# Optimization experiments

Hardware: AMD Instinct MI355X
Metric: run time of the kernel (lower is better)

Reference implementation:

```python
import jax, jax.numpy as jnp
import numpy as np

B, N, E, DIN = 2048, 38, 4, 9
H0, H1, L0 = 256, 256, 512
EPS = 1e-5
_mask_np = np.ones((N, DIN), np.float32)
_mask_np[np.arange(0, N, 2), :] = 0.0
MASK = jnp.asarray(_mask_np)  # (N, DIN); masked rows zeroed


def _bn_relu(h, g, b):
    # h: (B, N, 1, D); BatchNorm2d(N) normalizes over (batch, H=1, W=D) per node channel
    mu = jnp.mean(h, axis=(0, 2, 3), keepdims=True)
    var = jnp.var(h, axis=(0, 2, 3), keepdims=True)  # biased var, as torch BN
    h = (h - mu) * jax.lax.rsqrt(var + EPS) * g[None, :, None, None] + b[None, :, None, None]
    return jax.nn.relu(h)


def _gconv(adj, nodes, Ws, bs, We, be):
    # adj: (B, E, N, N); nodes: (B, N, 1, Din)
    out = Ws.shape[0]
    hs = nodes @ Ws.T + bs  # self term: (B, N, 1, out)
    m = (nodes @ We.T + be).reshape(nodes.shape[0], N, out, E)
    hr = jnp.einsum('bemn,bnce->bmc', adj, m)  # relational aggregation
    return hs + hr[:, :, None, :]


def _forward(adj, x, cWs0, cbs0, cWe0, cbe0, cg0, cb0, cWs1, cbs1, cWe1, cbe1, cg1, cb1, lW0, lb0, lg0, lbb0, fW, fb):
    masked_x = MASK * x
    h = masked_x[:, :, None, :]
    h = _bn_relu(_gconv(adj, h, cWs0, cbs0, cWe0, cbe0), cg0, cb0)
    h = _bn_relu(_gconv(adj, h, cWs1, cbs1, cWe1, cbe1), cg1, cb1)
    h = _bn_relu(h @ lW0.T + lb0, lg0, lbb0)
    h = (h @ fW.T + fb)[:, :, 0, :]  # (B, N, 2*DIN)
    s_logits, t = h[..., :DIN], h[..., DIN:]
    s = jax.nn.sigmoid(s_logits)
    out = masked_x + (1.0 - MASK) * (x + t) * s
    logdet = jnp.sum(jax.nn.log_sigmoid(s_logits).reshape(x.shape[0], -1), axis=1)
    return out, logdet


def setup_inputs() -> dict:
    key = jax.random.key(0)
    ks = jax.random.split(key, 8)
    rn = lambda k, shape: jax.random.normal(ks[k], shape, jnp.float32) * 0.1
    return {
        'adj': jax.random.uniform(ks[0], (B, E, N, N), jnp.float32),
        'x': jax.random.normal(ks[1], (B, N, DIN), jnp.float32),
        'cWs0': rn(2, (H0, DIN)), 'cbs0': jnp.zeros((H0,), jnp.float32),
        'cWe0': rn(3, (H0 * E, DIN)), 'cbe0': jnp.zeros((H0 * E,), jnp.float32),
        'cg0': jnp.ones((N,), jnp.float32), 'cb0': jnp.zeros((N,), jnp.float32),
        'cWs1': rn(4, (H1, H0)), 'cbs1': jnp.zeros((H1,), jnp.float32),
        'cWe1': rn(5, (H1 * E, H0)), 'cbe1': jnp.zeros((H1 * E,), jnp.float32),
        'cg1': jnp.ones((N,), jnp.float32), 'cb1': jnp.zeros((N,), jnp.float32),
        'lW0': rn(6, (L0, H1)), 'lb0': jnp.zeros((L0,), jnp.float32),
        'lg0': jnp.ones((N,), jnp.float32), 'lbb0': jnp.zeros((N,), jnp.float32),
        'fW': rn(7, (2 * DIN, L0)), 'fb': jnp.zeros((2 * DIN,), jnp.float32),
    }


def reference(adj, x, cWs0, cbs0, cWe0, cbe0, cg0, cb0, cWs1, cbs1, cWe1, cbe1, cg1, cb1, lW0, lb0, lg0, lbb0, fW, fb):
    return _forward(adj, x, cWs0, cbs0, cWe0, cbe0, cg0, cb0, cWs1, cbs1, cWe1, cbe1, cg1, cb1, lW0, lb0, lg0, lbb0, fW, fb)
```

## Files before the change

### kernel.cpp

```cpp
#include <hip/hip_runtime.h>
#include <hip/hip_bf16.h>
#include <math.h>

#define B_   2048
#define N_   38
#define E_   4
#define DIN_ 9
#define H0_  256
#define H1_  256
#define L0_  512
#define M_   (B_ * N_)

typedef short bf16x8 __attribute__((ext_vector_type(8)));
typedef float f32x4 __attribute__((ext_vector_type(4)));

__device__ __forceinline__ float b2f(unsigned short u) {
  return __uint_as_float((unsigned)u << 16);
}
__device__ __forceinline__ unsigned short f2b(float f) {
  __hip_bfloat16 h = __float2bfloat16(f);
  return *(unsigned short*)&h;
}

__device__ __forceinline__ float rsum16(float v) {
  v += __shfl_xor(v, 1);
  v += __shfl_xor(v, 2);
  v += __shfl_xor(v, 4);
  v += __shfl_xor(v, 8);
  return v;
}

__global__ void k_build_wg0(const float* __restrict__ Ws, const float* __restrict__ bs,
                            const float* __restrict__ We, const float* __restrict__ be,
                            unsigned short* __restrict__ WT) {
  int i = blockIdx.x * 256 + threadIdx.x;
  if (i >= 256 * 96) return;
  int c = i / 96, k = i % 96;
  float v = 0.f;
  if (k < 64) {
    int e = k >> 4, f = k & 15;
    if (f < 9) v = We[(c * 4 + e) * 9 + f];
    else if (f == 9) v = be[c * 4 + e];
  } else if (k < 80) {
    int f = k - 64;
    if (f < 9) v = Ws[c * 9 + f];
    else if (f == 9) v = bs[c];
  }
  WT[i] = f2b(v);
}

__global__ void k_build_wcat(const float* __restrict__ Ws, const float* __restrict__ We,
                             unsigned short* __restrict__ WT) {
  int i = blockIdx.x * 256 + threadIdx.x;
  if (i >= 256 * 1280) return;
  int c = i / 1280, k = i % 1280;
  float v;
  if (k < 256) v = Ws[c * 256 + k];
  else { int kk = k - 256; int e = kk >> 8, f = kk & 255; v = We[(c * 4 + e) * 256 + f]; }
  WT[i] = f2b(v);
}

__global__ void k_build_wl(const float* __restrict__ W, unsigned short* __restrict__ WT) {
  int i = blockIdx.x * 256 + threadIdx.x;
  if (i >= 512 * 256) return;
  WT[i] = f2b(W[i]);
}

__global__ void k_build_wf(const float* __restrict__ W, unsigned short* __restrict__ WT) {
  int i = blockIdx.x * 256 + threadIdx.x;
  if (i >= 32 * 512) return;
  int r = i / 512, k = i % 512;
  WT[i] = f2b(r < 18 ? W[r * 512 + k] : 0.f);
}

__global__ __launch_bounds__(256) void k_gred(const float* __restrict__ part, int nblk,
                                              float* __restrict__ st) {
  const int j = blockIdx.x, tid = threadIdx.x;
  float s = 0.f;
  for (int i = tid; i < nblk; i += 256) s += part[(size_t)i * 76 + j];
#pragma unroll
  for (int off = 32; off; off >>= 1) s += __shfl_down(s, off);
  __shared__ float r[4];
  if ((tid & 63) == 0) r[tid >> 6] = s;
  __syncthreads();
  if (tid == 0) {
    float tot = r[0] + r[1] + r[2] + r[3];
    if (j < 38) st[j * 2] = tot;
    else st[(j - 38) * 2 + 1] = tot;
  }
}

__global__ __launch_bounds__(256) void k_gconv0(
    const float* __restrict__ adj, const float* __restrict__ x,
    const unsigned short* __restrict__ Wg0, unsigned short* __restrict__ g,
    float* __restrict__ part) {
  __shared__ __align__(16) unsigned short adjB[4 * 48 * 64];
  __shared__ __align__(16) unsigned short zB[48 * 64];
  __shared__ __align__(16) unsigned short xLA[64 * 32];
  __shared__ __align__(16) unsigned short xLB[16 * 64];
  __shared__ float lsumW[4][48], lsqW[4][48];
  const int b = blockIdx.x, t = threadIdx.x;
  const uint4 z4 = make_uint4(0, 0, 0, 0);
  for (int i = t; i < 4 * 48 * 64 / 8; i += 256) ((uint4*)adjB)[i] = z4;
  for (int i = t; i < 64 * 32 / 8; i += 256) ((uint4*)xLA)[i] = z4;
  for (int i = t; i < 16 * 64 / 8; i += 256) ((uint4*)xLB)[i] = z4;
  __syncthreads();
  for (int i = t; i < 4 * 38 * 38; i += 256) {
    int e = i / 1444, r = i % 1444, m = r / 38, n = r % 38;
    adjB[(e * 48 + m) * 64 + n] = f2b(adj[(size_t)b * 5776 + i]);
  }
  for (int i = t; i < 342; i += 256) {
    int m = i / 9, f = i % 9;
    float v = x[(size_t)b * 342 + i];
    unsigned short bv = f2b((m & 1) ? v : 0.f);
    xLA[m * 32 + f] = bv;
    xLB[f * 64 + m] = bv;
  }
  if (t < 38) {
    unsigned short one = f2b(1.f);
    xLA[t * 32 + 9] = one;
    xLB[9 * 64 + t] = one;
  }
  __syncthreads();
  const int w = t >> 6, L = t & 63;
  const int lrow = L & 15, quad = L >> 4;
  {
    f32x4 za[3];
#pragma unroll
    for (int mt = 0; mt < 3; ++mt) za[mt] = (f32x4){0.f, 0.f, 0.f, 0.f};
#pragma unroll
    for (int kk = 0; kk < 2; ++kk) {
      bf16x8 bb = *(const bf16x8*)&xLB[lrow * 64 + kk * 32 + quad * 8];
#pragma unroll
      for (int mt = 0; mt < 3; ++mt) {
        bf16x8 aa = *(const bf16x8*)&adjB[(w * 48 + mt * 16 + lrow) * 64 + kk * 32 + quad * 8];
        za[mt] = __builtin_amdgcn_mfma_f32_16x16x32_bf16(aa, bb, za[mt], 0, 0, 0);
      }
    }
#pragma unroll
    for (int mt = 0; mt < 3; ++mt)
#pragma unroll
      for (int reg = 0; reg < 4; ++reg)
        zB[(mt * 16 + quad * 4 + reg) * 64 + w * 16 + lrow] = f2b(za[mt][reg]);
  }
  __syncthreads();
  f32x4 acc[3][4];
#pragma unroll
  for (int mt = 0; mt < 3; ++mt)
#pragma unroll
    for (int nt = 0; nt < 4; ++nt) acc[mt][nt] = (f32x4){0.f, 0.f, 0.f, 0.f};
#pragma unroll
  for (int kc = 0; kc < 3; ++kc) {
    bf16x8 af[3];
#pragma unroll
    for (int mt = 0; mt < 3; ++mt)
      af[mt] = (kc < 2)
                   ? *(const bf16x8*)&zB[(mt * 16 + lrow) * 64 + kc * 32 + quad * 8]
                   : *(const bf16x8*)&xLA[(mt * 16 + lrow) * 32 + quad * 8];
#pragma unroll
    for (int nt = 0; nt < 4; ++nt) {
      const int c = w * 64 + nt * 16 + lrow;
      bf16x8 bf_ = *(const bf16x8*)&Wg0[(size_t)c * 96 + kc * 32 + quad * 8];
#pragma unroll
      for (int mt = 0; mt < 3; ++mt)
        acc[mt][nt] = __builtin_amdgcn_mfma_f32_16x16x32_bf16(af[mt], bf_, acc[mt][nt], 0, 0, 0);
    }
  }
#pragma unroll
  for (int mt = 0; mt < 3; ++mt) {
#pragma unroll
    for (int reg = 0; reg < 4; ++reg) {
      const int m = mt * 16 + quad * 4 + reg;
      float sv = 0.f, qv = 0.f;
      if (m < N_) {
#pragma unroll
        for (int nt = 0; nt < 4; ++nt) {
          const int c = w * 64 + nt * 16 + lrow;
          float v = acc[mt][nt][reg];
          g[((size_t)b * N_ + m) * 256 + c] = f2b(v);
          sv += v;
          qv += v * v;
        }
      }
      sv = rsum16(sv);
      qv = rsum16(qv);
      if (lrow == 0) { lsumW[w][m] = sv; lsqW[w][m] = qv; }
    }
  }
  __syncthreads();
  if (t < 38) {
    part[(size_t)b * 76 + t] = lsumW[0][t] + lsumW[1][t] + lsumW[2][t] + lsumW[3][t];
    part[(size_t)b * 76 + 38 + t] = lsqW[0][t] + lsqW[1][t] + lsqW[2][t] + lsqW[3][t];
  }
}

__global__ __launch_bounds__(256) void k_l1f(
    const float* __restrict__ adj, const unsigned short* __restrict__ g0,
    const unsigned short* __restrict__ Wcat, const float* __restrict__ st0,
    const float* __restrict__ gam, const float* __restrict__ bet,
    const float* __restrict__ bs, const float* __restrict__ be,
    unsigned short* __restrict__ h2, float* __restrict__ part) {
  __shared__ __align__(16) unsigned short adjB[4 * 48 * 64];
  __shared__ __align__(16) unsigned short Abt[256 * 48 + 16];
  __shared__ __align__(16) unsigned short Pbuf[48 * 256];
  __shared__ float aS[38], bS[38];
  __shared__ float arowS[4 * 48];
  __shared__ float lsumW[4][48], lsqW[4][48];
  const int b = blockIdx.x, t = threadIdx.x;
  for (int i = t; i < 4 * 48 * 64 / 8; i += 256) ((uint4*)adjB)[i] = make_uint4(0, 0, 0, 0);
  if (t < 38) {
    const float cnt = 2048.f * 256.f;
    float mu = st0[t * 2] / cnt;
    float var = st0[t * 2 + 1] / cnt - mu * mu;
    float a = rsqrtf(var + 1e-5f) * gam[t];
    aS[t] = a;
    bS[t] = bet[t] - mu * a;
  }
  __syncthreads();
  for (int i = t; i < 4 * 38 * 38; i += 256) {
    int e = i / 1444, r = i % 1444, m = r / 38, n = r % 38;
    *(unsigned short*)((char*)adjB + (e * 48 + m) * 128 + ((2 * n) ^ ((m & 7) << 4))) =
        f2b(adj[(size_t)b * 5776 + i]);
  }
  for (int i = t; i < 38 * 32; i += 256) {
    int n = i >> 5, seg = (i & 31) * 8;
    uint4 u = *(const uint4*)&g0[((size_t)b * N_ + n) * 256 + seg];
    float a = aS[n], bb2 = bS[n];
    unsigned* up = (unsigned*)&u;
    uint4 o;
    unsigned* op = (unsigned*)&o;
#pragma unroll
    for (int j = 0; j < 4; ++j) {
      float lo = fmaxf(fmaf(b2f((unsigned short)(up[j] & 0xffff)), a, bb2), 0.f);
      float hi = fmaxf(fmaf(b2f((unsigned short)(up[j] >> 16)), a, bb2), 0.f);
      op[j] = (unsigned)f2b(lo) | ((unsigned)f2b(hi) << 16);
    }
    *(uint4*)((char*)Pbuf + n * 512 + ((seg * 2) ^ ((n & 7) << 4))) = o;
  }
  for (int i = t; i < 10 * 32; i += 256) {
    int n = 38 + (i >> 5), seg = (i & 31) * 8;
    *(uint4*)((char*)Pbuf + n * 512 + ((seg * 2) ^ ((n & 7) << 4))) = make_uint4(0, 0, 0, 0);
  }
  __syncthreads();
  if (t < 152) {
    int e = t / 38, m = t % 38;
    float s = 0.f;
    for (int n = 0; n < 38; ++n)
      s += b2f(*(const unsigned short*)((const char*)adjB + (e * 48 + m) * 128 +
                                        ((2 * n) ^ ((m & 7) << 4))));
    arowS[e * 48 + m] = s;
  }
  {
    const int c = t;
#pragma unroll
    for (int j = 0; j < 5; ++j) {
      uint4 o;
      unsigned* op = (unsigned*)&o;
#pragma unroll
      for (int q = 0; q < 4; ++q) {
        int n0 = j * 8 + q * 2;
        unsigned short lo = 0, hi = 0;
        if (n0 < 38)
          lo = *(const unsigned short*)((const char*)Pbuf + n0 * 512 +
                                        ((2 * c) ^ ((n0 & 7) << 4)));
        if (n0 + 1 < 38)
          hi = *(const unsigned short*)((const char*)Pbuf + (n0 + 1) * 512 +
                                        ((2 * c) ^ (((n0 + 1) & 7) << 4)));
        op[q] = (unsigned)lo | ((unsigned)hi << 16);
      }
      *(uint4*)&Abt[c * 48 + j * 8] = o;
    }
    *(uint4*)&Abt[c * 48 + 40] = make_uint4(0, 0, 0, 0);
  }
  const int w = t >> 6, L = t & 63;
  const int lrow = L & 15, quad = L >> 4;
  f32x4 acc[3][4];
#pragma unroll
  for (int mt = 0; mt < 3; ++mt)
#pragma unroll
    for (int nt = 0; nt < 4; ++nt) acc[mt][nt] = (f32x4){0.f, 0.f, 0.f, 0.f};

#define MAIN_KBLOCK(WOFF)                                                              \
  _Pragma("unroll") for (int kc = 0; kc < 8; ++kc) {                                   \
    bf16x8 af[3];                                                                      \
    _Pragma("unroll") for (int mt = 0; mt < 3; ++mt) af[mt] =                          \
        *(const bf16x8*)((const char*)Pbuf + (mt * 16 + lrow) * 512 +                  \
                         ((kc * 64 + quad * 16) ^ ((lrow & 7) << 4)));                 \
    _Pragma("unroll") for (int nt = 0; nt < 4; ++nt) {                                 \
      const int c = w * 64 + nt * 16 + lrow;                                           \
      bf16x8 bf_ = *(const bf16x8*)&Wcat[(size_t)c * 1280 + (WOFF) + kc * 32 + quad * 8]; \
      _Pragma("unroll") for (int mt = 0; mt < 3; ++mt) acc[mt][nt] =                   \
          __builtin_amdgcn_mfma_f32_16x16x32_bf16(af[mt], bf_, acc[mt][nt], 0, 0, 0);  \
    }                                                                                  \
  }

  MAIN_KBLOCK(0)

#pragma unroll 1
  for (int e = 0; e < 4; ++e) {
    f32x4 pa[3][4];
#pragma unroll
    for (int mt = 0; mt < 3; ++mt)
#pragma unroll
      for (int nt = 0; nt < 4; ++nt) pa[mt][nt] = (f32x4){0.f, 0.f, 0.f, 0.f};
#pragma unroll
    for (int kk = 0; kk < 2; ++kk) {
      bf16x8 bb[4];
#pragma unroll
      for (int nt = 0; nt < 4; ++nt)
        bb[nt] = *(const bf16x8*)&Abt[(w * 64 + nt * 16 + lrow) * 48 + kk * 32 + quad * 8];
#pragma unroll
      for (int mt = 0; mt < 3; ++mt) {
        bf16x8 aa = *(const bf16x8*)((const char*)adjB + (e * 48 + mt * 16 + lrow) * 128 +
                                     ((kk * 64 + quad * 16) ^ ((lrow & 7) << 4)));
#pragma unroll
        for (int nt = 0; nt < 4; ++nt)
          pa[mt][nt] = __builtin_amdgcn_mfma_f32_16x16x32_bf16(aa, bb[nt], pa[mt][nt], 0, 0, 0);
      }
    }
    __syncthreads();
#pragma unroll
    for (int mt = 0; mt < 3; ++mt)
#pragma unroll
      for (int reg = 0; reg < 4; ++reg) {
        const int m = mt * 16 + quad * 4 + reg;
#pragma unroll
        for (int nt = 0; nt < 4; ++nt) {
          const int c2 = w * 64 + nt * 16 + lrow;
          *(unsigned short*)((char*)Pbuf + m * 512 + ((2 * c2) ^ ((m & 7) << 4))) =
              f2b(pa[mt][nt][reg]);
        }
      }
    __syncthreads();
    MAIN_KBLOCK(256 + e * 256)
  }
#undef MAIN_KBLOCK

#pragma unroll
  for (int mt = 0; mt < 3; ++mt) {
#pragma unroll
    for (int reg = 0; reg < 4; ++reg) {
      const int m = mt * 16 + quad * 4 + reg;
      float sv = 0.f, qv = 0.f;
      if (m < N_) {
        float a0 = arowS[0 * 48 + m], a1 = arowS[48 + m];
        float a2 = arowS[96 + m], a3 = arowS[144 + m];
#pragma unroll
        for (int nt = 0; nt < 4; ++nt) {
          const int col = w * 64 + nt * 16 + lrow;
          float4 bev = *(const float4*)&be[col * 4];
          float v = acc[mt][nt][reg] + bs[col] +
                    a0 * bev.x + a1 * bev.y + a2 * bev.z + a3 * bev.w;
          h2[((size_t)b * N_ + m) * 256 + col] = f2b(v);
          sv += v;
          qv += v * v;
        }
      }
      sv = rsum16(sv);
      qv = rsum16(qv);
      if (lrow == 0) { lsumW[w][m] = sv; lsqW[w][m] = qv; }
    }
  }
  __syncthreads();
  if (t < 38) {
    part[(size_t)b * 76 + t] = lsumW[0][t] + lsumW[1][t] + lsumW[2][t] + lsumW[3][t];
    part[(size_t)b * 76 + 38 + t] = lsqW[0][t] + lsqW[1][t] + lsqW[2][t] + lsqW[3][t];
  }
}

template <bool BIAS, bool STATS>
__global__ __launch_bounds__(512) void k_gemm(
    const unsigned short* __restrict__ A0, const unsigned short* __restrict__ Bw,
    const float* __restrict__ bias, const float* __restrict__ stIn,
    const float* __restrict__ gam, const float* __restrict__ bet, float cnt,
    unsigned short* __restrict__ Cout, int Cstride, float* __restrict__ part) {
  __shared__ __align__(16) unsigned short lA[128 * 32];
  __shared__ __align__(16) unsigned short lB[256 * 32];
  __shared__ float lbias[256];
  __shared__ float lsum[38], lsq[38];
  const int t = threadIdx.x;
  const int tileM = blockIdx.x, n_base = blockIdx.y * 256;
  if (BIAS && t < 256) lbias[t] = bias[n_base + t];
  if (STATS && t < 38) { lsum[t] = 0.f; lsq[t] = 0.f; }
  const int w = t >> 6, L = t & 63;
  const int wr = w >> 2, wc = w & 3;
  const int lrow = L & 15, quad = L >> 4;
  const int srow = t >> 2, sseg = (t & 3) * 8;
  const int nA = (tileM * 128 + srow) % 38;
  float aC, bC;
  {
    float mu = stIn[nA * 2] / cnt;
    float var = stIn[nA * 2 + 1] / cnt - mu * mu;
    aC = rsqrtf(var + 1e-5f) * gam[nA];
    bC = bet[nA] - mu * aC;
  }
  const unsigned short* aRow = A0 + (size_t)(tileM * 128 + srow) * 256 + sseg;
  f32x4 acc[4][4];
#pragma unroll
  for (int mt = 0; mt < 4; ++mt)
#pragma unroll
    for (int nt = 0; nt < 4; ++nt) acc[mt][nt] = (f32x4){0.f, 0.f, 0.f, 0.f};

  uint4 u = *(const uint4*)aRow;
  for (int ki = 0; ki < 8; ++ki) {
#pragma unroll
    for (int r = 0; r < 2; ++r) {
      const unsigned short* gp = Bw + (size_t)(n_base + r * 128 + srow) * 256 + ki * 32 + sseg;
      __builtin_amdgcn_global_load_lds(
          (const __attribute__((address_space(1))) void*)gp,
          (__attribute__((address_space(3))) void*)(lB + r * 4096 + w * 512), 16, 0, 0);
    }
    uint4 un = u;
    if (ki < 7) un = *(const uint4*)(aRow + (ki + 1) * 32);
    {
      uint4 o;
      unsigned* up = (unsigned*)&u;
      unsigned* op = (unsigned*)&o;
#pragma unroll
      for (int j = 0; j < 4; ++j) {
        float lo = fmaxf(fmaf(b2f((unsigned short)(up[j] & 0xffff)), aC, bC), 0.f);
        float hi = fmaxf(fmaf(b2f((unsigned short)(up[j] >> 16)), aC, bC), 0.f);
        op[j] = (unsigned)f2b(lo) | ((unsigned)f2b(hi) << 16);
      }
      *(uint4*)&lA[srow * 32 + sseg] = o;
    }
    __syncthreads();
    bf16x8 af[4], bfr[4];
#pragma unroll
    for (int mt = 0; mt < 4; ++mt)
      af[mt] = *(const bf16x8*)&lA[(wr * 64 + mt * 16 + lrow) * 32 + quad * 8];
#pragma unroll
    for (int nt = 0; nt < 4; ++nt)
      bfr[nt] = *(const bf16x8*)&lB[(wc * 64 + nt * 16 + lrow) * 32 + quad * 8];
#pragma unroll
    for (int mt = 0; mt < 4; ++mt)
#pragma unroll
      for (int nt = 0; nt < 4; ++nt)
        acc[mt][nt] = __builtin_amdgcn_mfma_f32_16x16x32_bf16(af[mt], bfr[nt], acc[mt][nt], 0, 0, 0);
    __syncthreads();
    u = un;
  }
#pragma unroll
  for (int mt = 0; mt < 4; ++mt) {
#pragma unroll
    for (int reg = 0; reg < 4; ++reg) {
      const size_t row = (size_t)tileM * 128 + wr * 64 + mt * 16 + quad * 4 + reg;
      float sv = 0.f, qv = 0.f;
#pragma unroll
      for (int nt = 0; nt < 4; ++nt) {
        const int lcol = wc * 64 + nt * 16 + lrow;
        float v = acc[mt][nt][reg];
        if (BIAS) v += lbias[lcol];
        Cout[row * Cstride + n_base + lcol] = f2b(v);
        sv += v;
        qv += v * v;
      }
      if (STATS) {
        sv = rsum16(sv);
        qv = rsum16(qv);
        if (lrow == 0) {
          int n = (int)(row % 38);
          atomicAdd(&lsum[n], sv);
          atomicAdd(&lsq[n], qv);
        }
      }
    }
  }
  if (STATS) {
    __syncthreads();
    const int blk = blockIdx.y * gridDim.x + blockIdx.x;
    if (t < 38) {
      part[(size_t)blk * 76 + t] = lsum[t];
      part[(size_t)blk * 76 + 38 + t] = lsq[t];
    }
  }
}

__global__ __launch_bounds__(256) void k_final(
    const unsigned short* __restrict__ g2, const float* __restrict__ x,
    const unsigned short* __restrict__ Wfb, const float* __restrict__ fb,
    const float* __restrict__ st, const float* __restrict__ gam,
    const float* __restrict__ bet, float* __restrict__ out) {
  __shared__ __align__(16) unsigned short hA[48 * 520];
  __shared__ float lgS[48 * 20];
  __shared__ float aS[N_], bS[N_], fbS[20], red[4];
  const int b = blockIdx.x, tid = threadIdx.x;
  if (tid < N_) {
    const float cnt = 2048.f * 512.f;
    float mu = st[tid * 2] / cnt;
    float var = st[tid * 2 + 1] / cnt - mu * mu;
    float a = rsqrtf(var + 1e-5f) * gam[tid];
    aS[tid] = a;
    bS[tid] = bet[tid] - mu * a;
  }
  if (tid >= 64 && tid < 82) fbS[tid - 64] = fb[tid - 64];
  __syncthreads();
  for (int i = tid; i < N_ * 64; i += 256) {
    int n = i >> 6, seg = (i & 63) * 8;
    uint4 u = *(const uint4*)&g2[((size_t)b * N_ + n) * 512 + seg];
    float a = aS[n], bb = bS[n];
    float v[8];
    v[0] = b2f((unsigned short)(u.x & 0xffff)); v[1] = b2f((unsigned short)(u.x >> 16));
    v[2] = b2f((unsigned short)(u.y & 0xffff)); v[3] = b2f((unsigned short)(u.y >> 16));
    v[4] = b2f((unsigned short)(u.z & 0xffff)); v[5] = b2f((unsigned short)(u.z >> 16));
    v[6] = b2f((unsigned short)(u.w & 0xffff)); v[7] = b2f((unsigned short)(u.w >> 16));
#pragma unroll
    for (int j = 0; j < 8; ++j) v[j] = fmaxf(fmaf(v[j], a, bb), 0.f);
    uint4 o;
    o.x = (unsigned)f2b(v[0]) | ((unsigned)f2b(v[1]) << 16);
    o.y = (unsigned)f2b(v[2]) | ((unsigned)f2b(v[3]) << 16);
    o.z = (unsigned)f2b(v[4]) | ((unsigned)f2b(v[5]) << 16);
    o.w = (unsigned)f2b(v[6]) | ((unsigned)f2b(v[7]) << 16);
    *(uint4*)&hA[n * 520 + seg] = o;
  }
  for (int i = tid; i < 10 * 64; i += 256) {
    int n = 38 + (i >> 6), seg = (i & 63) * 8;
    *(uint4*)&hA[n * 520 + seg] = make_uint4(0, 0, 0, 0);
  }
  __syncthreads();
  const int w = tid >> 6, L = tid & 63;
  const int lrow = L & 15, quad = L >> 4;
  if (w < 3) {
    f32x4 acc0 = (f32x4){0.f, 0.f, 0.f, 0.f}, acc1 = (f32x4){0.f, 0.f, 0.f, 0.f};
#pragma unroll
    for (int ki = 0; ki < 16; ++ki) {
      bf16x8 af = *(const bf16x8*)&hA[(w * 16 + lrow) * 520 + ki * 32 + quad * 8];
      bf16x8 b0 = *(const bf16x8*)&Wfb[(size_t)lrow * 512 + ki * 32 + quad * 8];
      bf16x8 b1 = *(const bf16x8*)&Wfb[(size_t)(16 + lrow) * 512 + ki * 32 + quad * 8];
      acc0 = __builtin_amdgcn_mfma_f32_16x16x32_bf16(af, b0, acc0, 0, 0, 0);
      acc1 = __builtin_amdgcn_mfma_f32_16x16x32_bf16(af, b1, acc1, 0, 0, 0);
    }
#pragma unroll
    for (int reg = 0; reg < 4; ++reg) {
      int m = w * 16 + quad * 4 + reg;
      if (m < N_) {
        lgS[m * 20 + lrow] = acc0[reg] + fbS[lrow];
        if (lrow < 2) lgS[m * 20 + 16 + lrow] = acc1[reg] + fbS[16 + lrow];
      }
    }
  }
  __syncthreads();
  float ls = 0.f;
  for (int ii = tid; ii < 342; ii += 256) {
    int mm = ii / 9, d = ii % 9;
    float sl = lgS[mm * 20 + d];
    float tv = lgS[mm * 20 + 9 + d];
    float xv = x[((size_t)b * N_ + mm) * 9 + d];
    float sg = 1.f / (1.f + expf(-sl));
    float o = (mm & 1) ? xv : (xv + tv) * sg;
    out[((size_t)b * N_ + mm) * 9 + d] = o;
    ls += (sl >= 0.f) ? -log1pf(expf(-sl)) : (sl - log1pf(expf(sl)));
  }
#pragma unroll
  for (int off = 32; off; off >>= 1) ls += __shfl_down(ls, off);
  if (L == 0) red[w] = ls;
  __syncthreads();
  if (tid == 0) out[(size_t)B_ * 342 + b] = red[0] + red[1] + red[2] + red[3];
}

extern "C" void kernel_launch(void* const* d_in, const int* in_sizes, int n_in,
                              void* d_out, int out_size, void* d_ws, size_t ws_size,
                              hipStream_t stream) {
  (void)in_sizes; (void)n_in; (void)out_size; (void)ws_size;
  const float* adj  = (const float*)d_in[0];
  const float* x    = (const float*)d_in[1];
  const float* cWs0 = (const float*)d_in[2];
  const float* cbs0 = (const float*)d_in[3];
  const float* cWe0 = (const float*)d_in[4];
  const float* cbe0 = (const float*)d_in[5];
  const float* cg0  = (const float*)d_in[6];
  const float* cb0  = (const float*)d_in[7];
  const float* cWs1 = (const float*)d_in[8];
  const float* cbs1 = (const float*)d_in[9];
  const float* cWe1 = (const float*)d_in[10];
  const float* cbe1 = (const float*)d_in[11];
  const float* cg1  = (const float*)d_in[12];
  const float* cb1  = (const float*)d_in[13];
  const float* lW0  = (const float*)d_in[14];
  const float* lb0  = (const float*)d_in[15];
  const float* lg0  = (const float*)d_in[16];
  const float* lbb0 = (const float*)d_in[17];
  const float* fW   = (const float*)d_in[18];
  const float* fb   = (const float*)d_in[19];
  float* out = (float*)d_out;

  char* p = (char*)d_ws;
  float* stats = (float*)p;                     p += 1024;
  unsigned short* Wg0  = (unsigned short*)p;    p += 256 * 96 * 2;
  unsigned short* Wfb  = (unsigned short*)p;    p += 32 * 512 * 2;
  unsigned short* Wcat = (unsigned short*)p;    p += 256 * 1280 * 2;
  unsigned short* Wl   = (unsigned short*)p;    p += 512 * 256 * 2;
  float* part0 = (float*)p;                     p += 2048 * 76 * 4;
  float* part1 = (float*)p;                     p += 2048 * 76 * 4;
  float* part2 = (float*)p;                     p += 1216 * 76 * 4;
  unsigned short* g0   = (unsigned short*)p;    p += (size_t)M_ * 256 * 2;
  unsigned short* h2   = (unsigned short*)p;    p += (size_t)M_ * 256 * 2;
  unsigned short* g2   = (unsigned short*)p;

  float* st0 = stats;
  float* st1 = stats + 76;
  float* st2 = stats + 152;

  k_build_wg0<<<96, 256, 0, stream>>>(cWs0, cbs0, cWe0, cbe0, Wg0);
  k_build_wcat<<<1280, 256, 0, stream>>>(cWs1, cWe1, Wcat);
  k_build_wl<<<512, 256, 0, stream>>>(lW0, Wl);
  k_build_wf<<<64, 256, 0, stream>>>(fW, Wfb);

  k_gconv0<<<2048, 256, 0, stream>>>(adj, x, Wg0, g0, part0);
  k_gred<<<76, 256, 0, stream>>>(part0, 2048, st0);

  k_l1f<<<2048, 256, 0, stream>>>(adj, g0, Wcat, st0, cg0, cb0, cbs1, cbe1, h2, part1);
  k_gred<<<76, 256, 0, stream>>>(part1, 2048, st1);

  k_gemm<true, true><<<dim3(608, 2), 512, 0, stream>>>(
      h2, Wl, lb0, st1, cg1, cb1, 2048.f * 256.f, g2, 512, part2);
  k_gred<<<76, 256, 0, stream>>>(part2, 1216, st2);

  k_final<<<2048, 256, 0, stream>>>(g2, x, Wfb, fb, st2, lg0, lbb0, out);
}
```

Measured before the change: 454.6 us.

## Stage all aggregated features in one LDS buffer before a single fused GEMM

The layer-1 kernel now computes all four adjacency aggregations up front into one large shared-memory tile S (a 48x1280 bf16 concat of self features plus four per-edge aggregates). It then runs a single uninterrupted K=1280 MFMA GEMM against Wcat, removing the per-edge syncthreads pairs that sat between the aggregation and GEMM phases. Adjacency is staged into S's tail region (later overwritten by edge 3's aggregate), loaded as float2 pairs, and the Abt fragments are held in registers across all edges. The cost is much higher LDS use (launch_bounds(256,1)) and likely one block per CU, which lowers occupancy and the ability to hide global Wcat loads.

```diff
diff --git a/kernel.cpp b/kernel.cpp
--- a/kernel.cpp
+++ b/kernel.cpp
@@ -194,20 +194,23 @@
   }
 }
 
-__global__ __launch_bounds__(256) void k_l1f(
+__global__ __launch_bounds__(256, 1) void k_l1f(
     const float* __restrict__ adj, const unsigned short* __restrict__ g0,
     const unsigned short* __restrict__ Wcat, const float* __restrict__ st0,
     const float* __restrict__ gam, const float* __restrict__ bet,
     const float* __restrict__ bs, const float* __restrict__ be,
     unsigned short* __restrict__ h2, float* __restrict__ part) {
-  __shared__ __align__(16) unsigned short adjB[4 * 48 * 64];
+  __shared__ __align__(16) unsigned short S[48 * 1280];
   __shared__ __align__(16) unsigned short Abt[256 * 48 + 16];
-  __shared__ __align__(16) unsigned short Pbuf[48 * 256];
   __shared__ float aS[38], bS[38];
-  __shared__ float arowS[4 * 48];
+  __shared__ float arowS[4 * 38];
   __shared__ float lsumW[4][48], lsqW[4][48];
   const int b = blockIdx.x, t = threadIdx.x;
-  for (int i = t; i < 4 * 48 * 64 / 8; i += 256) ((uint4*)adjB)[i] = make_uint4(0, 0, 0, 0);
+  for (int i = t; i < 48 * 32; i += 256) {
+    int m = i >> 5, q = i & 31;
+    *(uint4*)((char*)S + m * 2560 + 2048 + q * 16) = make_uint4(0, 0, 0, 0);
+  }
+  if (t < 2) *(uint4*)&Abt[256 * 48 + t * 8] = make_uint4(0, 0, 0, 0);
   if (t < 38) {
     const float cnt = 2048.f * 256.f;
     float mu = st0[t * 2] / cnt;
@@ -217,10 +220,11 @@
     bS[t] = bet[t] - mu * a;
   }
   __syncthreads();
-  for (int i = t; i < 4 * 38 * 38; i += 256) {
-    int e = i / 1444, r = i % 1444, m = r / 38, n = r % 38;
-    *(unsigned short*)((char*)adjB + (e * 48 + m) * 128 + ((2 * n) ^ ((m & 7) << 4))) =
-        f2b(adj[(size_t)b * 5776 + i]);
+  for (int i = t; i < 4 * 38 * 19; i += 256) {
+    int e = i / 722, r = i % 722, m = r / 19, p2 = r % 19;
+    float2 v = *(const float2*)&adj[(size_t)b * 5776 + e * 1444 + m * 38 + 2 * p2];
+    unsigned pk = (unsigned)f2b(v.x) | ((unsigned)f2b(v.y) << 16);
+    *(unsigned*)((char*)S + m * 2560 + 2048 + e * 128 + ((4 * p2) ^ ((m & 7) << 4))) = pk;
   }
   for (int i = t; i < 38 * 32; i += 256) {
     int n = i >> 5, seg = (i & 31) * 8;
@@ -235,21 +239,9 @@
       float hi = fmaxf(fmaf(b2f((unsigned short)(up[j] >> 16)), a, bb2), 0.f);
       op[j] = (unsigned)f2b(lo) | ((unsigned)f2b(hi) << 16);
     }
-    *(uint4*)((char*)Pbuf + n * 512 + ((seg * 2) ^ ((n & 7) << 4))) = o;
-  }
-  for (int i = t; i < 10 * 32; i += 256) {
-    int n = 38 + (i >> 5), seg = (i & 31) * 8;
-    *(uint4*)((char*)Pbuf + n * 512 + ((seg * 2) ^ ((n & 7) << 4))) = make_uint4(0, 0, 0, 0);
-  }
-  __syncthreads();
-  if (t < 152) {
-    int e = t / 38, m = t % 38;
-    float s = 0.f;
-    for (int n = 0; n < 38; ++n)
-      s += b2f(*(const unsigned short*)((const char*)adjB + (e * 48 + m) * 128 +
-                                        ((2 * n) ^ ((m & 7) << 4))));
-    arowS[e * 48 + m] = s;
-  }
+    *(uint4*)((char*)S + n * 2560 + ((seg * 2) ^ ((n & 7) << 4))) = o;
+  }
+  __syncthreads();
   {
     const int c = t;
 #pragma unroll
@@ -261,10 +253,10 @@
         int n0 = j * 8 + q * 2;
         unsigned short lo = 0, hi = 0;
         if (n0 < 38)
-          lo = *(const unsigned short*)((const char*)Pbuf + n0 * 512 +
+          lo = *(const unsigned short*)((const char*)S + n0 * 2560 +
                                         ((2 * c) ^ ((n0 & 7) << 4)));
         if (n0 + 1 < 38)
-          hi = *(const unsigned short*)((const char*)Pbuf + (n0 + 1) * 512 +
+          hi = *(const unsigned short*)((const char*)S + (n0 + 1) * 2560 +
                                         ((2 * c) ^ (((n0 + 1) & 7) << 4)));
         op[q] = (unsigned)lo | ((unsigned)hi << 16);
       }
@@ -272,53 +264,41 @@
     }
     *(uint4*)&Abt[c * 48 + 40] = make_uint4(0, 0, 0, 0);
   }
+  if (t < 152) {
+    int e2 = t / 38, m2 = t % 38;
+    float s = 0.f;
+    for (int n = 0; n < 38; ++n)
+      s += b2f(*(const unsigned short*)((const char*)S + m2 * 2560 + 2048 + e2 * 128 +
+                                        ((2 * n) ^ ((m2 & 7) << 4))));
+    arowS[e2 * 38 + m2] = s;
+  }
+  __syncthreads();
   const int w = t >> 6, L = t & 63;
   const int lrow = L & 15, quad = L >> 4;
-  f32x4 acc[3][4];
-#pragma unroll
-  for (int mt = 0; mt < 3; ++mt)
-#pragma unroll
-    for (int nt = 0; nt < 4; ++nt) acc[mt][nt] = (f32x4){0.f, 0.f, 0.f, 0.f};
-
-#define MAIN_KBLOCK(WOFF)                                                              \
-  _Pragma("unroll") for (int kc = 0; kc < 8; ++kc) {                                   \
-    bf16x8 af[3];                                                                      \
-    _Pragma("unroll") for (int mt = 0; mt < 3; ++mt) af[mt] =                          \
-        *(const bf16x8*)((const char*)Pbuf + (mt * 16 + lrow) * 512 +                  \
-                         ((kc * 64 + quad * 16) ^ ((lrow & 7) << 4)));                 \
-    _Pragma("unroll") for (int nt = 0; nt < 4; ++nt) {                                 \
-      const int c = w * 64 + nt * 16 + lrow;                                           \
-      bf16x8 bf_ = *(const bf16x8*)&Wcat[(size_t)c * 1280 + (WOFF) + kc * 32 + quad * 8]; \
-      _Pragma("unroll") for (int mt = 0; mt < 3; ++mt) acc[mt][nt] =                   \
-          __builtin_amdgcn_mfma_f32_16x16x32_bf16(af[mt], bf_, acc[mt][nt], 0, 0, 0);  \
-    }                                                                                  \
-  }
-
-  MAIN_KBLOCK(0)
-
-#pragma unroll 1
-  for (int e = 0; e < 4; ++e) {
+  const int swzL = (lrow & 7) << 4;
+  bf16x8 bbr[2][4];
+#pragma unroll
+  for (int kk = 0; kk < 2; ++kk)
+#pragma unroll
+    for (int nt = 0; nt < 4; ++nt)
+      bbr[kk][nt] = *(const bf16x8*)&Abt[(w * 64 + nt * 16 + lrow) * 48 + kk * 32 + quad * 8];
+#pragma unroll
+  for (int e = 0; e < 3; ++e) {
     f32x4 pa[3][4];
 #pragma unroll
     for (int mt = 0; mt < 3; ++mt)
 #pragma unroll
       for (int nt = 0; nt < 4; ++nt) pa[mt][nt] = (f32x4){0.f, 0.f, 0.f, 0.f};
 #pragma unroll
-    for (int kk = 0; kk < 2; ++kk) {
-      bf16x8 bb[4];
-#pragma unroll
-      for (int nt = 0; nt < 4; ++nt)
-        bb[nt] = *(const bf16x8*)&Abt[(w * 64 + nt * 16 + lrow) * 48 + kk * 32 + quad * 8];
+    for (int kk = 0; kk < 2; ++kk)
 #pragma unroll
       for (int mt = 0; mt < 3; ++mt) {
-        bf16x8 aa = *(const bf16x8*)((const char*)adjB + (e * 48 + mt * 16 + lrow) * 128 +
-                                     ((kk * 64 + quad * 16) ^ ((lrow & 7) << 4)));
+        bf16x8 aa = *(const bf16x8*)((const char*)S + (mt * 16 + lrow) * 2560 + 2048 +
+                                     e * 128 + ((kk * 64 + quad * 16) ^ swzL));
 #pragma unroll
         for (int nt = 0; nt < 4; ++nt)
-          pa[mt][nt] = __builtin_amdgcn_mfma_f32_16x16x32_bf16(aa, bb[nt], pa[mt][nt], 0, 0, 0);
-      }
-    }
-    __syncthreads();
+          pa[mt][nt] = __builtin_amdgcn_mfma_f32_16x16x32_bf16(aa, bbr[kk][nt], pa[mt][nt], 0, 0, 0);
+      }
 #pragma unroll
     for (int mt = 0; mt < 3; ++mt)
 #pragma unroll
@@ -327,15 +307,63 @@
 #pragma unroll
         for (int nt = 0; nt < 4; ++nt) {
           const int c2 = w * 64 + nt * 16 + lrow;
-          *(unsigned short*)((char*)Pbuf + m * 512 + ((2 * c2) ^ ((m & 7) << 4))) =
-              f2b(pa[mt][nt][reg]);
+          *(unsigned short*)((char*)S + m * 2560 + 512 + e * 512 +
+                             ((2 * c2) ^ ((m & 7) << 4))) = f2b(pa[mt][nt][reg]);
         }
       }
-    __syncthreads();
-    MAIN_KBLOCK(256 + e * 256)
-  }
-#undef MAIN_KBLOCK
-
+  }
+  f32x4 pa3[3][4];
+#pragma unroll
+  for (int mt = 0; mt < 3; ++mt)
+#pragma unroll
+    for (int nt = 0; nt < 4; ++nt) pa3[mt][nt] = (f32x4){0.f, 0.f, 0.f, 0.f};
+#pragma unroll
+  for (int kk = 0; kk < 2; ++kk)
+#pragma unroll
+    for (int mt = 0; mt < 3; ++mt) {
+      bf16x8 aa = *(const bf16x8*)((const char*)S + (mt * 16 + lrow) * 2560 + 2048 +
+                                   3 * 128 + ((kk * 64 + quad * 16) ^ swzL));
+#pragma unroll
+      for (int nt = 0; nt < 4; ++nt)
+        pa3[mt][nt] = __builtin_amdgcn_mfma_f32_16x16x32_bf16(aa, bbr[kk][nt], pa3[mt][nt], 0, 0, 0);
+    }
+  __syncthreads();
+#pragma unroll
+  for (int mt = 0; mt < 3; ++mt)
+#pragma unroll
+    for (int reg = 0; reg < 4; ++reg) {
+      const int m = mt * 16 + quad * 4 + reg;
+#pragma unroll
+      for (int nt = 0; nt < 4; ++nt) {
+        const int c2 = w * 64 + nt * 16 + lrow;
+        *(unsigned short*)((char*)S + m * 2560 + 2048 +
+                           ((2 * c2) ^ ((m & 7) << 4))) = f2b(pa3[mt][nt][reg]);
+      }
+    }
+  __syncthreads();
+  f32x4 acc[3][4];
+#pragma unroll
+  for (int mt = 0; mt < 3; ++mt)
+#pragma unroll
+    for (int nt = 0; nt < 4; ++nt) acc[mt][nt] = (f32x4){0.f, 0.f, 0.f, 0.f};
+#pragma unroll
+  for (int kb = 0; kb < 5; ++kb)
+#pragma unroll
+    for (int kc = 0; kc < 8; ++kc) {
+      bf16x8 af[3];
+#pragma unroll
+      for (int mt = 0; mt < 3; ++mt)
+        af[mt] = *(const bf16x8*)((const char*)S + (mt * 16 + lrow) * 2560 +
+                                  ((kb * 512 + kc * 64 + quad * 16) ^ swzL));
+#pragma unroll
+      for (int nt = 0; nt < 4; ++nt) {
+        const int c = w * 64 + nt * 16 + lrow;
+        bf16x8 bf_ = *(const bf16x8*)&Wcat[(size_t)c * 1280 + kb * 256 + kc * 32 + quad * 8];
+#pragma unroll
+        for (int mt = 0; mt < 3; ++mt)
+          acc[mt][nt] = __builtin_amdgcn_mfma_f32_16x16x32_bf16(af[mt], bf_, acc[mt][nt], 0, 0, 0);
+      }
+    }
 #pragma unroll
   for (int mt = 0; mt < 3; ++mt) {
 #pragma unroll
@@ -343,8 +371,8 @@
       const int m = mt * 16 + quad * 4 + reg;
       float sv = 0.f, qv = 0.f;
       if (m < N_) {
-        float a0 = arowS[0 * 48 + m], a1 = arowS[48 + m];
-        float a2 = arowS[96 + m], a3 = arowS[144 + m];
+        float a0 = arowS[0 * 38 + m], a1 = arowS[38 + m];
+        float a2 = arowS[76 + m], a3 = arowS[114 + m];
 #pragma unroll
         for (int nt = 0; nt < 4; ++nt) {
           const int col = w * 64 + nt * 16 + lrow;
```

Result: slower. 538.8 us (+18.5%).

## Shrink k_l1f shared memory: compact adj layout, hold transposed P in registers

Applied to the files above, without the earlier changes.

Replaces the padded swizzled adjacency buffer with a compact 40x40 bf16 layout loaded via float2 vector reads, and drops the Abt transposed staging buffer. Each lane now gathers the transposed P fragments straight into registers once, and reuses them for all four edge types. Launch bounds now request three blocks per CU. Together these cut LDS use to raise occupancy, at the cost of more registers and scattered 2-byte LDS gathers. The padded-row masking logic for the adjacency fragments also adds some risk of correctness mistakes.

```diff
diff --git a/kernel.cpp b/kernel.cpp
--- a/kernel.cpp
+++ b/kernel.cpp
@@ -194,20 +194,19 @@
   }
 }
 
-__global__ __launch_bounds__(256) void k_l1f(
+__global__ __launch_bounds__(256, 3) void k_l1f(
     const float* __restrict__ adj, const unsigned short* __restrict__ g0,
     const unsigned short* __restrict__ Wcat, const float* __restrict__ st0,
     const float* __restrict__ gam, const float* __restrict__ bet,
     const float* __restrict__ bs, const float* __restrict__ be,
     unsigned short* __restrict__ h2, float* __restrict__ part) {
-  __shared__ __align__(16) unsigned short adjB[4 * 48 * 64];
-  __shared__ __align__(16) unsigned short Abt[256 * 48 + 16];
   __shared__ __align__(16) unsigned short Pbuf[48 * 256];
+  __shared__ __align__(16) unsigned short adjC[4 * 40 * 40];
   __shared__ float aS[38], bS[38];
-  __shared__ float arowS[4 * 48];
+  __shared__ float arowS[4 * 38];
   __shared__ float lsumW[4][48], lsqW[4][48];
   const int b = blockIdx.x, t = threadIdx.x;
-  for (int i = t; i < 4 * 48 * 64 / 8; i += 256) ((uint4*)adjB)[i] = make_uint4(0, 0, 0, 0);
+  for (int i = t; i < 800; i += 256) ((uint4*)adjC)[i] = make_uint4(0, 0, 0, 0);
   if (t < 38) {
     const float cnt = 2048.f * 256.f;
     float mu = st0[t * 2] / cnt;
@@ -217,10 +216,11 @@
     bS[t] = bet[t] - mu * a;
   }
   __syncthreads();
-  for (int i = t; i < 4 * 38 * 38; i += 256) {
-    int e = i / 1444, r = i % 1444, m = r / 38, n = r % 38;
-    *(unsigned short*)((char*)adjB + (e * 48 + m) * 128 + ((2 * n) ^ ((m & 7) << 4))) =
-        f2b(adj[(size_t)b * 5776 + i]);
+  for (int i = t; i < 4 * 38 * 19; i += 256) {
+    int e = i / 722, r = i % 722, m = r / 19, p2 = r % 19;
+    float2 v = *(const float2*)&adj[(size_t)b * 5776 + e * 1444 + m * 38 + 2 * p2];
+    unsigned pk = (unsigned)f2b(v.x) | ((unsigned)f2b(v.y) << 16);
+    *(unsigned*)&adjC[(e * 40 + m) * 40 + 2 * p2] = pk;
   }
   for (int i = t; i < 38 * 32; i += 256) {
     int n = i >> 5, seg = (i & 31) * 8;
@@ -242,38 +242,38 @@
     *(uint4*)((char*)Pbuf + n * 512 + ((seg * 2) ^ ((n & 7) << 4))) = make_uint4(0, 0, 0, 0);
   }
   __syncthreads();
-  if (t < 152) {
-    int e = t / 38, m = t % 38;
-    float s = 0.f;
-    for (int n = 0; n < 38; ++n)
-      s += b2f(*(const unsigned short*)((const char*)adjB + (e * 48 + m) * 128 +
-                                        ((2 * n) ^ ((m & 7) << 4))));
-    arowS[e * 48 + m] = s;
-  }
-  {
-    const int c = t;
-#pragma unroll
-    for (int j = 0; j < 5; ++j) {
-      uint4 o;
-      unsigned* op = (unsigned*)&o;
-#pragma unroll
-      for (int q = 0; q < 4; ++q) {
-        int n0 = j * 8 + q * 2;
-        unsigned short lo = 0, hi = 0;
-        if (n0 < 38)
-          lo = *(const unsigned short*)((const char*)Pbuf + n0 * 512 +
-                                        ((2 * c) ^ ((n0 & 7) << 4)));
-        if (n0 + 1 < 38)
-          hi = *(const unsigned short*)((const char*)Pbuf + (n0 + 1) * 512 +
-                                        ((2 * c) ^ (((n0 + 1) & 7) << 4)));
-        op[q] = (unsigned)lo | ((unsigned)hi << 16);
-      }
-      *(uint4*)&Abt[c * 48 + j * 8] = o;
-    }
-    *(uint4*)&Abt[c * 48 + 40] = make_uint4(0, 0, 0, 0);
-  }
   const int w = t >> 6, L = t & 63;
   const int lrow = L & 15, quad = L >> 4;
+  const int swzL = (lrow & 7) << 4;
+  bf16x8 bbr[2][4];
+#pragma unroll
+  for (int kk = 0; kk < 2; ++kk)
+#pragma unroll
+    for (int nt = 0; nt < 4; ++nt) {
+      const int c2 = 2 * (w * 64 + nt * 16 + lrow);
+      unsigned pk[4];
+#pragma unroll
+      for (int jp = 0; jp < 4; ++jp) {
+        int n0 = kk * 32 + quad * 8 + 2 * jp;
+        int na = n0 < 48 ? n0 : 47;
+        int nb = (n0 + 1) < 48 ? (n0 + 1) : 47;
+        unsigned short lo =
+            *(const unsigned short*)((const char*)Pbuf + na * 512 + (c2 ^ ((na & 7) << 4)));
+        unsigned short hi =
+            *(const unsigned short*)((const char*)Pbuf + nb * 512 + (c2 ^ ((nb & 7) << 4)));
+        pk[jp] = (unsigned)lo | ((unsigned)hi << 16);
+      }
+      union { unsigned u[4]; bf16x8 v; } uu;
+      uu.u[0] = pk[0]; uu.u[1] = pk[1]; uu.u[2] = pk[2]; uu.u[3] = pk[3];
+      bbr[kk][nt] = uu.v;
+    }
+  if (t < 152) {
+    int e2 = t / 38, m2 = t % 38;
+    float s = 0.f;
+    for (int n = 0; n < 38; ++n) s += b2f(adjC[(e2 * 40 + m2) * 40 + n]);
+    arowS[e2 * 38 + m2] = s;
+  }
+
   f32x4 acc[3][4];
 #pragma unroll
   for (int mt = 0; mt < 3; ++mt)
@@ -285,7 +285,7 @@
     bf16x8 af[3];                                                                      \
     _Pragma("unroll") for (int mt = 0; mt < 3; ++mt) af[mt] =                          \
         *(const bf16x8*)((const char*)Pbuf + (mt * 16 + lrow) * 512 +                  \
-                         ((kc * 64 + quad * 16) ^ ((lrow & 7) << 4)));                 \
+                         ((kc * 64 + quad * 16) ^ swzL));                              \
     _Pragma("unroll") for (int nt = 0; nt < 4; ++nt) {                                 \
       const int c = w * 64 + nt * 16 + lrow;                                           \
       bf16x8 bf_ = *(const bf16x8*)&Wcat[(size_t)c * 1280 + (WOFF) + kc * 32 + quad * 8]; \
@@ -305,17 +305,17 @@
       for (int nt = 0; nt < 4; ++nt) pa[mt][nt] = (f32x4){0.f, 0.f, 0.f, 0.f};
 #pragma unroll
     for (int kk = 0; kk < 2; ++kk) {
-      bf16x8 bb[4];
-#pragma unroll
-      for (int nt = 0; nt < 4; ++nt)
-        bb[nt] = *(const bf16x8*)&Abt[(w * 64 + nt * 16 + lrow) * 48 + kk * 32 + quad * 8];
 #pragma unroll
       for (int mt = 0; mt < 3; ++mt) {
-        bf16x8 aa = *(const bf16x8*)((const char*)adjB + (e * 48 + mt * 16 + lrow) * 128 +
-                                     ((kk * 64 + quad * 16) ^ ((lrow & 7) << 4)));
+        const int ma = mt * 16 + lrow;
+        const int mr = ma < 40 ? ma : 0;
+        const int cb = (kk == 0) ? (quad * 8) : (quad == 0 ? 32 : 0);
+        bf16x8 aa = *(const bf16x8*)&adjC[(e * 40 + mr) * 40 + cb];
+        const bool okf = (ma < 40) && (kk == 0 || quad == 0);
+        if (!okf) aa = (bf16x8){0, 0, 0, 0, 0, 0, 0, 0};
 #pragma unroll
         for (int nt = 0; nt < 4; ++nt)
-          pa[mt][nt] = __builtin_amdgcn_mfma_f32_16x16x32_bf16(aa, bb[nt], pa[mt][nt], 0, 0, 0);
+          pa[mt][nt] = __builtin_amdgcn_mfma_f32_16x16x32_bf16(aa, bbr[kk][nt], pa[mt][nt], 0, 0, 0);
       }
     }
     __syncthreads();
@@ -343,8 +343,8 @@
       const int m = mt * 16 + quad * 4 + reg;
       float sv = 0.f, qv = 0.f;
       if (m < N_) {
-        float a0 = arowS[0 * 48 + m], a1 = arowS[48 + m];
-        float a2 = arowS[96 + m], a3 = arowS[144 + m];
+        float a0 = arowS[0 * 38 + m], a1 = arowS[38 + m];
+        float a2 = arowS[76 + m], a3 = arowS[114 + m];
 #pragma unroll
         for (int nt = 0; nt < 4; ++nt) {
           const int col = w * 64 + nt * 16 + lrow;
```

Measured after the change: 555.8 us. 22.3% more time.
